# Kernel optimization log

Hardware: AMD Instinct MI355X
Metric: run time of the kernel (lower is better)

## Reference

```python
import jax, jax.numpy as jnp
import numpy as np

N, M, D, O = 16384, 4096, 256, 256

def setup_inputs() -> dict:
    key = jax.random.key(0)
    k1, k2, k3, k4, k5, k6, k7 = jax.random.split(key, 7)
    H_fine = jax.random.normal(k1, (N, D), dtype=jnp.float32)
    H_coarse = jax.random.normal(k2, (M, D), dtype=jnp.float32)
    inter_channel_adj = jax.random.randint(k3, (N, M), 0, 2).astype(jnp.float32)
    # attention = nn.Linear(2D, 1): weight vector [2D], bias scalar
    wa = jax.random.normal(k4, (2 * D,), dtype=jnp.float32) * (1.0 / np.sqrt(2 * D))
    ba = jax.random.normal(k5, (1,), dtype=jnp.float32) * 0.01
    # transform = nn.Linear(D, O), xavier_uniform weight
    lim = np.sqrt(6.0 / (D + O)).astype(np.float32)
    Wt = jax.random.uniform(k6, (O, D), minval=-lim, maxval=lim, dtype=jnp.float32)
    bt = jax.random.normal(k7, (O,), dtype=jnp.float32) * 0.01
    return {"H_fine": H_fine, "H_coarse": H_coarse,
            "inter_channel_adj": inter_channel_adj,
            "wa": wa, "ba": ba, "Wt": Wt, "bt": bt}

def reference(H_fine, H_coarse, inter_channel_adj, wa, ba, Wt, bt):
    d = H_fine.shape[-1]
    # additive attention: score_ij = [hf_i ; hc_j] . wa + b
    # = hf_i . wa[:d] + hc_j . wa[d:] + b  (avoids [N,M,2D] concat)
    sf = H_fine @ wa[:d]            # [N]
    sc = H_coarse @ wa[d:]          # [M]
    scores = sf[:, None] + sc[None, :] + ba[0]        # [N, M]
    masked = scores * inter_channel_adj               # [N, M]
    weights = jax.nn.softmax(masked, axis=-1)         # [N, M]
    attn_out = weights @ H_coarse                     # [N, D]
    attn_out = attn_out + H_fine                      # add_self=True
    out = attn_out @ Wt.T + bt                        # [N, O]
    return jax.nn.relu(out)
```

## Files before the change

kernel.cpp:

```cpp
#include <hip/hip_runtime.h>
#include <hip/hip_bf16.h>
#include <stdint.h>

#define N_ 16384
#define M_ 4096
#define D_ 256
#define O_ 256

#define WS_T    0
#define WS_U    65536
#define WS_R    81920
#define WS_LSUM 98304
#define WS_WTP  163840
#define WS_BP   294912
#define WS_CP   2457600
#define WS_ABF  20971520

typedef float  f32x4  __attribute__((ext_vector_type(4)));
typedef short  short8 __attribute__((ext_vector_type(8)));
typedef unsigned short ushortx4 __attribute__((ext_vector_type(4)));

__device__ __forceinline__ unsigned short f2bf(float f) {
  uint32_t u = __float_as_uint(f);
  u += 0x7FFFu + ((u >> 16) & 1u);
  return (unsigned short)(u >> 16);
}
__device__ __forceinline__ uint32_t cvtpk(float a, float b) {
  __hip_bfloat162 h = __float22bfloat162_rn(float2{a, b});
  uint32_t u;
  __builtin_memcpy(&u, &h, 4);
  return u;
}
__device__ __forceinline__ float bf2f(unsigned short v) {
  return __uint_as_float((uint32_t)v << 16);
}

__global__ __launch_bounds__(256) void rowdot_exp_kernel(
    const float* __restrict__ X, const float* __restrict__ w,
    const float* __restrict__ bias, float* __restrict__ outv) {
  int wv = threadIdx.x >> 6, lane = threadIdx.x & 63;
  int row = blockIdx.x * 4 + wv;
  const float4* x4 = (const float4*)(X + (size_t)row * D_);
  const float4* w4 = (const float4*)w;
  float4 xa = x4[lane], wa4 = w4[lane];
  float s = xa.x * wa4.x + xa.y * wa4.y + xa.z * wa4.z + xa.w * wa4.w;
#pragma unroll
  for (int off = 32; off > 0; off >>= 1) s += __shfl_xor(s, off);
  if (lane == 0) outv[row] = expf(s + (bias ? bias[0] : 0.0f));
}

__global__ __launch_bounds__(256) void hc_pack_kernel(
    const float* __restrict__ Hc, unsigned short* __restrict__ BP,
    float* __restrict__ R) {
  __shared__ float tile[64][65];
  __shared__ float red[4][64];
  int bk = blockIdx.x >> 2;
  int bc = blockIdx.x & 3;
  int k0 = bk * 64, col0 = bc * 64;
  int t = threadIdx.x;
  int lane = t & 63, wv = t >> 6;
  int m = lane & 15, q = lane >> 4;
  float colsum = 0.0f;
#pragma unroll
  for (int i = 0; i < 16; ++i) {
    int e = t + 256 * i;
    int kk = e >> 6, cc = e & 63;
    float v = Hc[(size_t)(k0 + kk) * D_ + col0 + cc];
    tile[kk][cc] = v;
    colsum += v;
  }
  red[wv][t & 63] = colsum;
  __syncthreads();
  if (t < 64)
    atomicAdd(&R[col0 + t], red[0][t] + red[1][t] + red[2][t] + red[3][t]);
#pragma unroll
  for (int t8 = 0; t8 < 2; ++t8) {
    int tile_id = t8 * 4 + wv;
    int sub = tile_id >> 2, g = tile_id & 3;
    int kgg = bk * 2 + sub;
    int cgg = bc * 4 + g;
    short8 v8;
#pragma unroll
    for (int j = 0; j < 8; ++j)
      v8[j] = (short)f2bf(tile[sub * 32 + q * 8 + j][g * 16 + m]);
    *(short8*)(BP + ((size_t)(kgg * 16 + cgg) * 64 + lane) * 8) = v8;
  }
}

__global__ __launch_bounds__(256) void wt_pack_kernel(
    const float* __restrict__ Wt, unsigned short* __restrict__ WtP) {
  int t = blockIdx.x * 256 + threadIdx.x;
  int lane = t & 63, cg = (t >> 6) & 15, kg = t >> 10;
  int m = lane & 15, q = lane >> 4;
  const float* src = Wt + (size_t)(cg * 16 + m) * D_ + kg * 32 + q * 8;
  float4 w0 = *(const float4*)src, w1 = *(const float4*)(src + 4);
  short8 v8;
  v8[0] = (short)f2bf(w0.x); v8[1] = (short)f2bf(w0.y);
  v8[2] = (short)f2bf(w0.z); v8[3] = (short)f2bf(w0.w);
  v8[4] = (short)f2bf(w1.x); v8[5] = (short)f2bf(w1.y);
  v8[6] = (short)f2bf(w1.z); v8[7] = (short)f2bf(w1.w);
  *(short8*)(WtP + (size_t)t * 8) = v8;
}

__global__ __launch_bounds__(512, 2) void pack_bits_kernel(
    const float* __restrict__ adj, const float* __restrict__ tv,
    const float* __restrict__ uv, unsigned char* __restrict__ ABF,
    float* __restrict__ Lsum) {
  __shared__ float u_lds[M_];
  __shared__ float redu[8][32];
  __shared__ float redc[8][32];
  int tid = threadIdx.x;
  int w = tid >> 6, lane = tid & 63;
  int q = lane >> 4, m = lane & 15;
  int b = blockIdx.x;
  int r0 = b * 32;

  for (int i = tid; i < M_; i += 512) u_lds[i] = uv[i];

  const float* a0 = adj + (size_t)(r0 + m) * M_ + q * 8;
  const float* a1 = a0 + (size_t)16 * M_;
  unsigned char* o0 = ABF + ((size_t)(2 * b) * 128) * 64 + lane;
  unsigned char* o1 = o0 + (size_t)128 * 64;
  float su0 = 0.f, sc0 = 0.f, su1 = 0.f, sc1 = 0.f;
  __syncthreads();

  int ks0 = w;
  float4 pa0 = *(const float4*)(a0 + ks0 * 32);
  float4 pa1 = *(const float4*)(a0 + ks0 * 32 + 4);
  float4 pb0 = *(const float4*)(a1 + ks0 * 32);
  float4 pb1 = *(const float4*)(a1 + ks0 * 32 + 4);

  for (int i = 0; i < 16; ++i) {
    int ks = w + 8 * i;
    int kn = (i + 1 < 16) ? ks + 8 : w;
    float4 na0 = *(const float4*)(a0 + kn * 32);
    float4 na1 = *(const float4*)(a0 + kn * 32 + 4);
    float4 nb0 = *(const float4*)(a1 + kn * 32);
    float4 nb1 = *(const float4*)(a1 + kn * 32 + 4);

    float4 u0 = *(const float4*)&u_lds[ks * 32 + q * 8];
    float4 u1 = *(const float4*)&u_lds[ks * 32 + q * 8 + 4];
    float A[8] = {pa0.x, pa0.y, pa0.z, pa0.w, pa1.x, pa1.y, pa1.z, pa1.w};
    float B[8] = {pb0.x, pb0.y, pb0.z, pb0.w, pb1.x, pb1.y, pb1.z, pb1.w};
    float U[8] = {u0.x, u0.y, u0.z, u0.w, u1.x, u1.y, u1.z, u1.w};
    uint32_t bits0 = 0, bits1 = 0;
#pragma unroll
    for (int j = 0; j < 8; ++j) {
      bits0 |= (A[j] != 0.0f ? 1u : 0u) << j;
      bits1 |= (B[j] != 0.0f ? 1u : 0u) << j;
      su0 = fmaf(A[j], U[j], su0);  sc0 += A[j];
      su1 = fmaf(B[j], U[j], su1);  sc1 += B[j];
    }
    o0[(size_t)ks * 64] = (unsigned char)bits0;
    o1[(size_t)ks * 64] = (unsigned char)bits1;
    pa0 = na0; pa1 = na1; pb0 = nb0; pb1 = nb1;
  }

  su0 += __shfl_xor(su0, 16); su0 += __shfl_xor(su0, 32);
  sc0 += __shfl_xor(sc0, 16); sc0 += __shfl_xor(sc0, 32);
  su1 += __shfl_xor(su1, 16); su1 += __shfl_xor(su1, 32);
  sc1 += __shfl_xor(sc1, 16); sc1 += __shfl_xor(sc1, 32);
  if (lane < 16) {
    redu[w][m] = su0;      redc[w][m] = sc0;
    redu[w][16 + m] = su1; redc[w][16 + m] = sc1;
  }
  __syncthreads();
  if (tid < 32) {
    float Su = 0.f, Sc = 0.f;
#pragma unroll
    for (int ww = 0; ww < 8; ++ww) { Su += redu[ww][tid]; Sc += redc[ww][tid]; }
    Lsum[r0 + tid] = tv[r0 + tid] * Su - Sc;
  }
}

__device__ __forceinline__ short8 frag_bits(uint32_t bits, float t,
                                            float4 u0, float4 u1) {
  float c[8];
  c[0] = fmaf(t, u0.x, -1.0f); c[1] = fmaf(t, u0.y, -1.0f);
  c[2] = fmaf(t, u0.z, -1.0f); c[3] = fmaf(t, u0.w, -1.0f);
  c[4] = fmaf(t, u1.x, -1.0f); c[5] = fmaf(t, u1.y, -1.0f);
  c[6] = fmaf(t, u1.z, -1.0f); c[7] = fmaf(t, u1.w, -1.0f);
  union { short8 s; uint32_t u[4]; } r;
#pragma unroll
  for (int p = 0; p < 4; ++p) {
    uint32_t mlo = 0u - ((bits >> (2 * p)) & 1u);
    uint32_t mhi = 0u - ((bits >> (2 * p + 1)) & 1u);
    r.u[p] = cvtpk(c[2 * p], c[2 * p + 1]) &
             ((mlo & 0x0000FFFFu) | (mhi & 0xFFFF0000u));
  }
  return r.s;
}

__global__ __launch_bounds__(256, 4) void main_kernel(
    const unsigned char* __restrict__ ABF, const unsigned short* __restrict__ BP,
    const float* __restrict__ tv, const float* __restrict__ uv,
    unsigned short* __restrict__ Cp) {
  __shared__ float u_lds[2048];
  int tid = threadIdx.x;
  int w = tid >> 6, lane = tid & 63;
  int q = lane >> 4, m = lane & 15;
  int bid = blockIdx.x;
  int kh = bid & 1, rb = bid >> 1;
  int c0 = w * 64;

  for (int i = tid; i < 2048; i += 256) u_lds[i] = uv[kh * 2048 + i];

  float t0 = tv[rb * 32 + m], t1 = tv[rb * 32 + 16 + m];
  const unsigned char* g0 =
      ABF + ((size_t)(2 * rb) * 128 + kh * 64) * 64 + lane;
  const unsigned char* g1 = g0 + (size_t)128 * 64;
  const unsigned short* bb =
      BP + ((size_t)(kh * 64) * 16 + w * 4) * 512 + (size_t)lane * 8;

  f32x4 acc[2][4];
#pragma unroll
  for (int s = 0; s < 2; ++s)
#pragma unroll
    for (int n = 0; n < 4; ++n) acc[s][n] = (f32x4){0.f, 0.f, 0.f, 0.f};

  __syncthreads();

  uint32_t xb0 = g0[0], xb1 = g1[0];
  uint32_t yb0 = g0[64], yb1 = g1[64];
  short8 BX[4], BY[4];
#pragma unroll
  for (int n = 0; n < 4; ++n) BX[n] = *(const short8*)(bb + n * 512);
#pragma unroll
  for (int n = 0; n < 4; ++n) BY[n] = *(const short8*)(bb + 8192 + n * 512);

  for (int kk = 0; kk < 64; kk += 2) {
    {
      int k2 = (kk + 2) & 63;
      uint32_t nb0 = g0[(size_t)k2 * 64], nb1 = g1[(size_t)k2 * 64];
      short8 nB[4];
#pragma unroll
      for (int n = 0; n < 4; ++n)
        nB[n] = *(const short8*)(bb + (size_t)k2 * 8192 + n * 512);
      float4 u0 = *(const float4*)&u_lds[kk * 32 + q * 8];
      float4 u1 = *(const float4*)&u_lds[kk * 32 + q * 8 + 4];
      short8 af0 = frag_bits(xb0, t0, u0, u1);
      short8 af1 = frag_bits(xb1, t1, u0, u1);
#pragma unroll
      for (int n = 0; n < 4; ++n) {
        acc[0][n] = __builtin_amdgcn_mfma_f32_16x16x32_bf16(af0, BX[n], acc[0][n], 0, 0, 0);
        acc[1][n] = __builtin_amdgcn_mfma_f32_16x16x32_bf16(af1, BX[n], acc[1][n], 0, 0, 0);
      }
      xb0 = nb0; xb1 = nb1;
#pragma unroll
      for (int n = 0; n < 4; ++n) BX[n] = nB[n];
    }
    {
      int k3 = (kk + 3) & 63;
      uint32_t nb0 = g0[(size_t)k3 * 64], nb1 = g1[(size_t)k3 * 64];
      short8 nB[4];
#pragma unroll
      for (int n = 0; n < 4; ++n)
        nB[n] = *(const short8*)(bb + (size_t)k3 * 8192 + n * 512);
      float4 u0 = *(const float4*)&u_lds[(kk + 1) * 32 + q * 8];
      float4 u1 = *(const float4*)&u_lds[(kk + 1) * 32 + q * 8 + 4];
      short8 af0 = frag_bits(yb0, t0, u0, u1);
      short8 af1 = frag_bits(yb1, t1, u0, u1);
#pragma unroll
      for (int n = 0; n < 4; ++n) {
        acc[0][n] = __builtin_amdgcn_mfma_f32_16x16x32_bf16(af0, BY[n], acc[0][n], 0, 0, 0);
        acc[1][n] = __builtin_amdgcn_mfma_f32_16x16x32_bf16(af1, BY[n], acc[1][n], 0, 0, 0);
      }
      yb0 = nb0; yb1 = nb1;
#pragma unroll
      for (int n = 0; n < 4; ++n) BY[n] = nB[n];
    }
  }

#pragma unroll
  for (int s = 0; s < 2; ++s)
#pragma unroll
    for (int n = 0; n < 4; ++n) {
      int col = c0 + n * 16 + m;
#pragma unroll
      for (int r = 0; r < 4; ++r) {
        size_t row = (size_t)rb * 32 + s * 16 + q * 4 + r;
        Cp[((size_t)kh * N_ + row) * D_ + col] = f2bf(acc[s][n][r]);
      }
    }
}

__global__ __launch_bounds__(256, 4) void epilogue_kernel(
    const unsigned short* __restrict__ Cp, const float* __restrict__ Lsum,
    const float* __restrict__ Rv, const float* __restrict__ Hf,
    const unsigned short* __restrict__ WtP, const float* __restrict__ bt,
    float* __restrict__ out) {
  __shared__ alignas(16) unsigned short attn[32][264];
  int tid = threadIdx.x;
  int w = tid >> 6, lane = tid & 63;
  int rtile = w & 1, chalf = w >> 1;
  int q = lane >> 4, m = lane & 15;
  int i0 = blockIdx.x * 32;

  float4 rv = *(const float4*)(Rv + lane * 4);
#pragma unroll
  for (int rr = 0; rr < 8; ++rr) {
    int r = w * 8 + rr;
    size_t row = (size_t)i0 + r;
    float invL = 1.0f / (Lsum[row] + (float)M_);
    ushortx4 cA = *(const ushortx4*)(Cp + row * D_ + lane * 4);
    ushortx4 cB = *(const ushortx4*)(Cp + ((size_t)N_ + row) * D_ + lane * 4);
    float4 hv = *(const float4*)(Hf + row * D_ + lane * 4);
    attn[r][lane * 4 + 0] = f2bf(fmaf(bf2f(cA[0]) + bf2f(cB[0]) + rv.x, invL, hv.x));
    attn[r][lane * 4 + 1] = f2bf(fmaf(bf2f(cA[1]) + bf2f(cB[1]) + rv.y, invL, hv.y));
    attn[r][lane * 4 + 2] = f2bf(fmaf(bf2f(cA[2]) + bf2f(cB[2]) + rv.z, invL, hv.z));
    attn[r][lane * 4 + 3] = f2bf(fmaf(bf2f(cA[3]) + bf2f(cB[3]) + rv.w, invL, hv.w));
  }
  __syncthreads();

  f32x4 facc[8];
#pragma unroll
  for (int n = 0; n < 8; ++n) facc[n] = (f32x4){0.f, 0.f, 0.f, 0.f};
  const unsigned short* wwave = WtP + (size_t)chalf * 4096 + (size_t)lane * 8;
#pragma unroll
  for (int kf = 0; kf < 8; ++kf) {
    short8 af = *(const short8*)&attn[rtile * 16 + m][kf * 32 + q * 8];
#pragma unroll
    for (int n = 0; n < 8; ++n) {
      short8 bf = *(const short8*)(wwave + ((size_t)kf * 16 + n) * 512);
      facc[n] = __builtin_amdgcn_mfma_f32_16x16x32_bf16(af, bf, facc[n], 0, 0, 0);
    }
  }
#pragma unroll
  for (int n = 0; n < 8; ++n) {
    int col = chalf * 128 + n * 16 + m;
    float b = bt[col];
#pragma unroll
    for (int r = 0; r < 4; ++r) {
      size_t row = (size_t)i0 + rtile * 16 + q * 4 + r;
      out[row * O_ + col] = fmaxf(facc[n][r] + b, 0.0f);
    }
  }
}

extern "C" void kernel_launch(void* const* d_in, const int* in_sizes, int n_in,
                              void* d_out, int out_size, void* d_ws, size_t ws_size,
                              hipStream_t stream) {
  const float* Hf  = (const float*)d_in[0];
  const float* Hc  = (const float*)d_in[1];
  const float* adj = (const float*)d_in[2];
  const float* wa  = (const float*)d_in[3];
  const float* ba  = (const float*)d_in[4];
  const float* Wt  = (const float*)d_in[5];
  const float* bt  = (const float*)d_in[6];
  float* out = (float*)d_out;

  char* ws = (char*)d_ws;
  float* tv   = (float*)(ws + WS_T);
  float* uv   = (float*)(ws + WS_U);
  float* Rv   = (float*)(ws + WS_R);
  float* Lsum = (float*)(ws + WS_LSUM);
  unsigned short* WtP = (unsigned short*)(ws + WS_WTP);
  unsigned short* BP  = (unsigned short*)(ws + WS_BP);
  unsigned short* Cp  = (unsigned short*)(ws + WS_CP);
  unsigned char*  ABF = (unsigned char*)(ws + WS_ABF);

  hipMemsetAsync(Rv, 0, D_ * sizeof(float), stream);

  rowdot_exp_kernel<<<N_ / 4, 256, 0, stream>>>(Hf, wa, ba, tv);
  rowdot_exp_kernel<<<M_ / 4, 256, 0, stream>>>(Hc, wa + D_, nullptr, uv);
  hc_pack_kernel<<<256, 256, 0, stream>>>(Hc, BP, Rv);
  wt_pack_kernel<<<32, 256, 0, stream>>>(Wt, WtP);

  pack_bits_kernel<<<N_ / 32, 512, 0, stream>>>(adj, tv, uv, ABF, Lsum);
  main_kernel<<<1024, 256, 0, stream>>>(ABF, BP, tv, uv, Cp);
  epilogue_kernel<<<N_ / 32, 256, 0, stream>>>(Cp, Lsum, Rv, Hf, WtP, bt, out);
}
```

Measured before the change: 490.3 us.

## Pack adjacency bits with wave ballots and retile GEMM into 64-row blocks

The bit-packing kernel now uses __ballot so each wave packs two full adjacency rows into 64-bit words, replacing the per-lane byte writes and the cross-wave LDS reduction. The main GEMM becomes a 1024-thread block over 64 rows that stages the whole row bitmask tile in LDS. Its 16 waves split columns four ways and K four ways, so each B fragment load feeds four row tiles. This trades the old 2-way K split for a 4-way split, so Cp partial-sum traffic doubles and the epilogue now reads four partials. Large blocks with big LDS use may also limit occupancy.

```diff
diff --git a/kernel.cpp b/kernel.cpp
--- a/kernel.cpp
+++ b/kernel.cpp
@@ -13,8 +13,8 @@
 #define WS_LSUM 98304
 #define WS_WTP  163840
 #define WS_BP   294912
-#define WS_CP   2457600
-#define WS_ABF  20971520
+#define WS_ABM  2457600
+#define WS_CP   10846208
 
 typedef float  f32x4  __attribute__((ext_vector_type(4)));
 typedef short  short8 __attribute__((ext_vector_type(8)));
@@ -102,74 +102,63 @@
   *(short8*)(WtP + (size_t)t * 8) = v8;
 }
 
-__global__ __launch_bounds__(512, 2) void pack_bits_kernel(
+__global__ __launch_bounds__(256) void pack_bits_kernel(
     const float* __restrict__ adj, const float* __restrict__ tv,
-    const float* __restrict__ uv, unsigned char* __restrict__ ABF,
+    const float* __restrict__ uv, unsigned long long* __restrict__ ABM,
     float* __restrict__ Lsum) {
   __shared__ float u_lds[M_];
-  __shared__ float redu[8][32];
-  __shared__ float redc[8][32];
   int tid = threadIdx.x;
   int w = tid >> 6, lane = tid & 63;
-  int q = lane >> 4, m = lane & 15;
-  int b = blockIdx.x;
-  int r0 = b * 32;
-
-  for (int i = tid; i < M_; i += 512) u_lds[i] = uv[i];
-
-  const float* a0 = adj + (size_t)(r0 + m) * M_ + q * 8;
-  const float* a1 = a0 + (size_t)16 * M_;
-  unsigned char* o0 = ABF + ((size_t)(2 * b) * 128) * 64 + lane;
-  unsigned char* o1 = o0 + (size_t)128 * 64;
-  float su0 = 0.f, sc0 = 0.f, su1 = 0.f, sc1 = 0.f;
+  for (int i = tid; i < M_; i += 256) u_lds[i] = uv[i];
   __syncthreads();
-
-  int ks0 = w;
-  float4 pa0 = *(const float4*)(a0 + ks0 * 32);
-  float4 pa1 = *(const float4*)(a0 + ks0 * 32 + 4);
-  float4 pb0 = *(const float4*)(a1 + ks0 * 32);
-  float4 pb1 = *(const float4*)(a1 + ks0 * 32 + 4);
-
+  int r0 = (blockIdx.x * 4 + w) * 2;
+  const float* arA = adj + (size_t)r0 * M_;
+  const float* arB = arA + M_;
+  float suA = 0.f, scA = 0.f, suB = 0.f, scB = 0.f;
+
+  float a0 = arA[lane], a1 = arA[64 + lane], a2 = arA[128 + lane], a3 = arA[192 + lane];
+  float b0 = arB[lane], b1 = arB[64 + lane], b2 = arB[128 + lane], b3 = arB[192 + lane];
+#pragma unroll 1
   for (int i = 0; i < 16; ++i) {
-    int ks = w + 8 * i;
-    int kn = (i + 1 < 16) ? ks + 8 : w;
-    float4 na0 = *(const float4*)(a0 + kn * 32);
-    float4 na1 = *(const float4*)(a0 + kn * 32 + 4);
-    float4 nb0 = *(const float4*)(a1 + kn * 32);
-    float4 nb1 = *(const float4*)(a1 + kn * 32 + 4);
-
-    float4 u0 = *(const float4*)&u_lds[ks * 32 + q * 8];
-    float4 u1 = *(const float4*)&u_lds[ks * 32 + q * 8 + 4];
-    float A[8] = {pa0.x, pa0.y, pa0.z, pa0.w, pa1.x, pa1.y, pa1.z, pa1.w};
-    float B[8] = {pb0.x, pb0.y, pb0.z, pb0.w, pb1.x, pb1.y, pb1.z, pb1.w};
-    float U[8] = {u0.x, u0.y, u0.z, u0.w, u1.x, u1.y, u1.z, u1.w};
-    uint32_t bits0 = 0, bits1 = 0;
-#pragma unroll
-    for (int j = 0; j < 8; ++j) {
-      bits0 |= (A[j] != 0.0f ? 1u : 0u) << j;
-      bits1 |= (B[j] != 0.0f ? 1u : 0u) << j;
-      su0 = fmaf(A[j], U[j], su0);  sc0 += A[j];
-      su1 = fmaf(B[j], U[j], su1);  sc1 += B[j];
-    }
-    o0[(size_t)ks * 64] = (unsigned char)bits0;
-    o1[(size_t)ks * 64] = (unsigned char)bits1;
-    pa0 = na0; pa1 = na1; pb0 = nb0; pb1 = nb1;
-  }
-
-  su0 += __shfl_xor(su0, 16); su0 += __shfl_xor(su0, 32);
-  sc0 += __shfl_xor(sc0, 16); sc0 += __shfl_xor(sc0, 32);
-  su1 += __shfl_xor(su1, 16); su1 += __shfl_xor(su1, 32);
-  sc1 += __shfl_xor(sc1, 16); sc1 += __shfl_xor(sc1, 32);
-  if (lane < 16) {
-    redu[w][m] = su0;      redc[w][m] = sc0;
-    redu[w][16 + m] = su1; redc[w][16 + m] = sc1;
-  }
-  __syncthreads();
-  if (tid < 32) {
-    float Su = 0.f, Sc = 0.f;
-#pragma unroll
-    for (int ww = 0; ww < 8; ++ww) { Su += redu[ww][tid]; Sc += redc[ww][tid]; }
-    Lsum[r0 + tid] = tv[r0 + tid] * Su - Sc;
+    int k0 = i * 256;
+    int k1 = (i + 1 < 16) ? k0 + 256 : 0;
+    float na0 = arA[k1 + lane],       na1 = arA[k1 + 64 + lane];
+    float na2 = arA[k1 + 128 + lane], na3 = arA[k1 + 192 + lane];
+    float nb0 = arB[k1 + lane],       nb1 = arB[k1 + 64 + lane];
+    float nb2 = arB[k1 + 128 + lane], nb3 = arB[k1 + 192 + lane];
+
+    unsigned long long wA0 = __ballot(a0 != 0.0f), wA1 = __ballot(a1 != 0.0f);
+    unsigned long long wA2 = __ballot(a2 != 0.0f), wA3 = __ballot(a3 != 0.0f);
+    unsigned long long wB0 = __ballot(b0 != 0.0f), wB1 = __ballot(b1 != 0.0f);
+    unsigned long long wB2 = __ballot(b2 != 0.0f), wB3 = __ballot(b3 != 0.0f);
+    suA = fmaf(a0, u_lds[k0 + lane], suA);
+    suA = fmaf(a1, u_lds[k0 + 64 + lane], suA);
+    suA = fmaf(a2, u_lds[k0 + 128 + lane], suA);
+    suA = fmaf(a3, u_lds[k0 + 192 + lane], suA);
+    scA += (a0 + a1) + (a2 + a3);
+    suB = fmaf(b0, u_lds[k0 + lane], suB);
+    suB = fmaf(b1, u_lds[k0 + 64 + lane], suB);
+    suB = fmaf(b2, u_lds[k0 + 128 + lane], suB);
+    suB = fmaf(b3, u_lds[k0 + 192 + lane], suB);
+    scB += (b0 + b1) + (b2 + b3);
+    if (lane < 8) {
+      int sel = lane & 3;
+      unsigned long long vA = sel == 0 ? wA0 : sel == 1 ? wA1 : sel == 2 ? wA2 : wA3;
+      unsigned long long vB = sel == 0 ? wB0 : sel == 1 ? wB1 : sel == 2 ? wB2 : wB3;
+      int r = (lane < 4) ? r0 : r0 + 1;
+      ABM[(size_t)r * 64 + i * 4 + sel] = (lane < 4) ? vA : vB;
+    }
+    a0 = na0; a1 = na1; a2 = na2; a3 = na3;
+    b0 = nb0; b1 = nb1; b2 = nb2; b3 = nb3;
+  }
+#pragma unroll
+  for (int off = 32; off > 0; off >>= 1) {
+    suA += __shfl_xor(suA, off); scA += __shfl_xor(scA, off);
+    suB += __shfl_xor(suB, off); scB += __shfl_xor(scB, off);
+  }
+  if (lane == 0) {
+    Lsum[r0] = tv[r0] * suA - scA;
+    Lsum[r0 + 1] = tv[r0 + 1] * suB - scB;
   }
 }
 
@@ -191,95 +180,79 @@
   return r.s;
 }
 
-__global__ __launch_bounds__(256, 4) void main_kernel(
-    const unsigned char* __restrict__ ABF, const unsigned short* __restrict__ BP,
+__global__ __launch_bounds__(1024, 4) void gemm_kernel(
+    const unsigned int* __restrict__ ABM32, const unsigned short* __restrict__ BP,
     const float* __restrict__ tv, const float* __restrict__ uv,
     unsigned short* __restrict__ Cp) {
-  __shared__ float u_lds[2048];
+  __shared__ unsigned int bt2[64][129];
+  __shared__ float u_lds[M_];
   int tid = threadIdx.x;
   int w = tid >> 6, lane = tid & 63;
   int q = lane >> 4, m = lane & 15;
-  int bid = blockIdx.x;
-  int kh = bid & 1, rb = bid >> 1;
-  int c0 = w * 64;
-
-  for (int i = tid; i < 2048; i += 256) u_lds[i] = uv[kh * 2048 + i];
-
-  float t0 = tv[rb * 32 + m], t1 = tv[rb * 32 + 16 + m];
-  const unsigned char* g0 =
-      ABF + ((size_t)(2 * rb) * 128 + kh * 64) * 64 + lane;
-  const unsigned char* g1 = g0 + (size_t)128 * 64;
-  const unsigned short* bb =
-      BP + ((size_t)(kh * 64) * 16 + w * 4) * 512 + (size_t)lane * 8;
-
-  f32x4 acc[2][4];
-#pragma unroll
-  for (int s = 0; s < 2; ++s)
+  int colq = w >> 2, ksub = w & 3;
+  int i0 = blockIdx.x * 64;
+
+  const unsigned short* bbase = BP + (size_t)(colq * 4) * 512 + (size_t)lane * 8;
+  int kg0 = ksub * 32;
+  short8 curB[4];
+#pragma unroll
+  for (int n = 0; n < 4; ++n)
+    curB[n] = *(const short8*)(bbase + ((size_t)kg0 * 16 + n) * 512);
+  float t0 = tv[i0 + m], t1 = tv[i0 + 16 + m];
+  float t2 = tv[i0 + 32 + m], t3 = tv[i0 + 48 + m];
+
+  for (int i = tid; i < M_; i += 1024) u_lds[i] = uv[i];
+  for (int p = tid; p < 8192; p += 1024) {
+    int row = p >> 7, word = p & 127;
+    bt2[row][word] = ABM32[(size_t)(i0 + row) * 128 + word];
+  }
+
+  f32x4 acc[4][4];
+#pragma unroll
+  for (int s = 0; s < 4; ++s)
 #pragma unroll
     for (int n = 0; n < 4; ++n) acc[s][n] = (f32x4){0.f, 0.f, 0.f, 0.f};
 
   __syncthreads();
 
-  uint32_t xb0 = g0[0], xb1 = g1[0];
-  uint32_t yb0 = g0[64], yb1 = g1[64];
-  short8 BX[4], BY[4];
-#pragma unroll
-  for (int n = 0; n < 4; ++n) BX[n] = *(const short8*)(bb + n * 512);
-#pragma unroll
-  for (int n = 0; n < 4; ++n) BY[n] = *(const short8*)(bb + 8192 + n * 512);
-
-  for (int kk = 0; kk < 64; kk += 2) {
-    {
-      int k2 = (kk + 2) & 63;
-      uint32_t nb0 = g0[(size_t)k2 * 64], nb1 = g1[(size_t)k2 * 64];
-      short8 nB[4];
-#pragma unroll
-      for (int n = 0; n < 4; ++n)
-        nB[n] = *(const short8*)(bb + (size_t)k2 * 8192 + n * 512);
-      float4 u0 = *(const float4*)&u_lds[kk * 32 + q * 8];
-      float4 u1 = *(const float4*)&u_lds[kk * 32 + q * 8 + 4];
-      short8 af0 = frag_bits(xb0, t0, u0, u1);
-      short8 af1 = frag_bits(xb1, t1, u0, u1);
-#pragma unroll
-      for (int n = 0; n < 4; ++n) {
-        acc[0][n] = __builtin_amdgcn_mfma_f32_16x16x32_bf16(af0, BX[n], acc[0][n], 0, 0, 0);
-        acc[1][n] = __builtin_amdgcn_mfma_f32_16x16x32_bf16(af1, BX[n], acc[1][n], 0, 0, 0);
-      }
-      xb0 = nb0; xb1 = nb1;
-#pragma unroll
-      for (int n = 0; n < 4; ++n) BX[n] = nB[n];
-    }
-    {
-      int k3 = (kk + 3) & 63;
-      uint32_t nb0 = g0[(size_t)k3 * 64], nb1 = g1[(size_t)k3 * 64];
-      short8 nB[4];
-#pragma unroll
-      for (int n = 0; n < 4; ++n)
-        nB[n] = *(const short8*)(bb + (size_t)k3 * 8192 + n * 512);
-      float4 u0 = *(const float4*)&u_lds[(kk + 1) * 32 + q * 8];
-      float4 u1 = *(const float4*)&u_lds[(kk + 1) * 32 + q * 8 + 4];
-      short8 af0 = frag_bits(yb0, t0, u0, u1);
-      short8 af1 = frag_bits(yb1, t1, u0, u1);
-#pragma unroll
-      for (int n = 0; n < 4; ++n) {
-        acc[0][n] = __builtin_amdgcn_mfma_f32_16x16x32_bf16(af0, BY[n], acc[0][n], 0, 0, 0);
-        acc[1][n] = __builtin_amdgcn_mfma_f32_16x16x32_bf16(af1, BY[n], acc[1][n], 0, 0, 0);
-      }
-      yb0 = nb0; yb1 = nb1;
-#pragma unroll
-      for (int n = 0; n < 4; ++n) BY[n] = nB[n];
-    }
-  }
-
-#pragma unroll
-  for (int s = 0; s < 2; ++s)
+  for (int it = 0; it < 32; ++it) {
+    int kg = kg0 + it;
+    int kn = (it + 1 < 32) ? kg + 1 : kg0;
+    short8 nB[4];
+#pragma unroll
+    for (int n = 0; n < 4; ++n)
+      nB[n] = *(const short8*)(bbase + ((size_t)kn * 16 + n) * 512);
+
+    float4 u0 = *(const float4*)&u_lds[kg * 32 + q * 8];
+    float4 u1 = *(const float4*)&u_lds[kg * 32 + q * 8 + 4];
+    uint32_t b0 = bt2[m][kg],      b1 = bt2[16 + m][kg];
+    uint32_t b2 = bt2[32 + m][kg], b3 = bt2[48 + m][kg];
+    int sh = q * 8;
+    short8 af0 = frag_bits((b0 >> sh) & 0xffu, t0, u0, u1);
+    short8 af1 = frag_bits((b1 >> sh) & 0xffu, t1, u0, u1);
+    short8 af2 = frag_bits((b2 >> sh) & 0xffu, t2, u0, u1);
+    short8 af3 = frag_bits((b3 >> sh) & 0xffu, t3, u0, u1);
 #pragma unroll
     for (int n = 0; n < 4; ++n) {
-      int col = c0 + n * 16 + m;
+      acc[0][n] = __builtin_amdgcn_mfma_f32_16x16x32_bf16(af0, curB[n], acc[0][n], 0, 0, 0);
+      acc[1][n] = __builtin_amdgcn_mfma_f32_16x16x32_bf16(af1, curB[n], acc[1][n], 0, 0, 0);
+      acc[2][n] = __builtin_amdgcn_mfma_f32_16x16x32_bf16(af2, curB[n], acc[2][n], 0, 0, 0);
+      acc[3][n] = __builtin_amdgcn_mfma_f32_16x16x32_bf16(af3, curB[n], acc[3][n], 0, 0, 0);
+    }
+#pragma unroll
+    for (int n = 0; n < 4; ++n) curB[n] = nB[n];
+  }
+
+  unsigned short* cpb = Cp + (size_t)ksub * N_ * D_;
+#pragma unroll
+  for (int s = 0; s < 4; ++s)
+#pragma unroll
+    for (int n = 0; n < 4; ++n) {
+      int col = colq * 64 + n * 16 + m;
 #pragma unroll
       for (int r = 0; r < 4; ++r) {
-        size_t row = (size_t)rb * 32 + s * 16 + q * 4 + r;
-        Cp[((size_t)kh * N_ + row) * D_ + col] = f2bf(acc[s][n][r]);
+        size_t row = (size_t)i0 + s * 16 + q * 4 + r;
+        cpb[row * D_ + col] = f2bf(acc[s][n][r]);
       }
     }
 }
@@ -302,13 +275,19 @@
     int r = w * 8 + rr;
     size_t row = (size_t)i0 + r;
     float invL = 1.0f / (Lsum[row] + (float)M_);
-    ushortx4 cA = *(const ushortx4*)(Cp + row * D_ + lane * 4);
-    ushortx4 cB = *(const ushortx4*)(Cp + ((size_t)N_ + row) * D_ + lane * 4);
+    ushortx4 c0 = *(const ushortx4*)(Cp + row * D_ + lane * 4);
+    ushortx4 c1 = *(const ushortx4*)(Cp + ((size_t)N_ + row) * D_ + lane * 4);
+    ushortx4 c2 = *(const ushortx4*)(Cp + ((size_t)2 * N_ + row) * D_ + lane * 4);
+    ushortx4 c3 = *(const ushortx4*)(Cp + ((size_t)3 * N_ + row) * D_ + lane * 4);
     float4 hv = *(const float4*)(Hf + row * D_ + lane * 4);
-    attn[r][lane * 4 + 0] = f2bf(fmaf(bf2f(cA[0]) + bf2f(cB[0]) + rv.x, invL, hv.x));
-    attn[r][lane * 4 + 1] = f2bf(fmaf(bf2f(cA[1]) + bf2f(cB[1]) + rv.y, invL, hv.y));
-    attn[r][lane * 4 + 2] = f2bf(fmaf(bf2f(cA[2]) + bf2f(cB[2]) + rv.z, invL, hv.z));
-    attn[r][lane * 4 + 3] = f2bf(fmaf(bf2f(cA[3]) + bf2f(cB[3]) + rv.w, invL, hv.w));
+    float s0 = (bf2f(c0[0]) + bf2f(c1[0])) + (bf2f(c2[0]) + bf2f(c3[0]));
+    float s1 = (bf2f(c0[1]) + bf2f(c1[1])) + (bf2f(c2[1]) + bf2f(c3[1]));
+    float s2 = (bf2f(c0[2]) + bf2f(c1[2])) + (bf2f(c2[2]) + bf2f(c3[2]));
+    float s3 = (bf2f(c0[3]) + bf2f(c1[3])) + (bf2f(c2[3]) + bf2f(c3[3]));
+    attn[r][lane * 4 + 0] = f2bf(fmaf(s0 + rv.x, invL, hv.x));
+    attn[r][lane * 4 + 1] = f2bf(fmaf(s1 + rv.y, invL, hv.y));
+    attn[r][lane * 4 + 2] = f2bf(fmaf(s2 + rv.z, invL, hv.z));
+    attn[r][lane * 4 + 3] = f2bf(fmaf(s3 + rv.w, invL, hv.w));
   }
   __syncthreads();
 
@@ -356,8 +335,8 @@
   float* Lsum = (float*)(ws + WS_LSUM);
   unsigned short* WtP = (unsigned short*)(ws + WS_WTP);
   unsigned short* BP  = (unsigned short*)(ws + WS_BP);
+  unsigned long long* ABM = (unsigned long long*)(ws + WS_ABM);
   unsigned short* Cp  = (unsigned short*)(ws + WS_CP);
-  unsigned char*  ABF = (unsigned char*)(ws + WS_ABF);
 
   hipMemsetAsync(Rv, 0, D_ * sizeof(float), stream);
 
@@ -366,7 +345,7 @@
   hc_pack_kernel<<<256, 256, 0, stream>>>(Hc, BP, Rv);
   wt_pack_kernel<<<32, 256, 0, stream>>>(Wt, WtP);
 
-  pack_bits_kernel<<<N_ / 32, 512, 0, stream>>>(adj, tv, uv, ABF, Lsum);
-  main_kernel<<<1024, 256, 0, stream>>>(ABF, BP, tv, uv, Cp);
+  pack_bits_kernel<<<2048, 256, 0, stream>>>(adj, tv, uv, ABM, Lsum);
+  gemm_kernel<<<N_ / 64, 1024, 0, stream>>>((const unsigned int*)ABM, BP, tv, uv, Cp);
   epilogue_kernel<<<N_ / 32, 256, 0, stream>>>(Cp, Lsum, Rv, Hf, WtP, bt, out);
 }
```

Measured after the change: 489.2 us. No clear change (-0.2%).
